# Performance work log

Hardware: AMD Instinct MI355X
Metric: run time of the kernel (lower is better)

## Reference

```python
import jax, jax.numpy as jnp
import numpy as np

N_R = 20          # cfg['n_r']
H = 0.01          # cfg['h'] integration step
ALPHA_N = 0.1     # alpha(D_s_n, R_s_n) folded scale (stable: |eig(H*matAn)| << 2.8)
ALPHA_P = 0.08    # alpha(D_s_p, R_s_p)
BETA_N = -0.5     # -beta(...) for negative electrode
BETA_P = 0.4      # beta(...) for positive electrode


def _make_mats():
    n = N_R - 1
    # FDM tridiagonal (1,-2,1) radial diffusion stencil (spm_model.matA)
    matA = (jnp.diag(-2.0 * jnp.ones(n))
            + jnp.diag(jnp.ones(n - 1), 1)
            + jnp.diag(jnp.ones(n - 1), -1)).astype(jnp.float32)
    # boundary-flux input vector (spm_model.matB): only surface node driven
    matB = jnp.zeros(n, jnp.float32).at[-1].set(1.0)
    matAn = ALPHA_N * matA
    matBn = ALPHA_N * BETA_N * matB
    matAp = ALPHA_P * matA
    matBp = ALPHA_P * BETA_P * matB
    return matAn, matBn, matAp, matBp


def setup_inputs() -> dict:
    key = jax.random.key(0)
    k1, k2 = jax.random.split(key)
    n = N_R - 1
    B, K = 4096, 1024
    x = jax.random.normal(k1, (B, 2 * n), jnp.float32)
    i_seq = jax.random.normal(k2, (B, K), jnp.float32)
    matAn, matBn, matAp, matBp = _make_mats()
    return {"x": x, "i_seq": i_seq,
            "matAn": matAn, "matBn": matBn,
            "matAp": matAp, "matBp": matBp,
            "k": K}


def _rk4_step(x, i_col, A, Bv):
    # f(x) = A @ x + B * i  (batched: x [B,n], i_col [B,1], Bv [n])
    def f(y):
        return y @ A.T + i_col * Bv
    k1 = f(x)
    k2 = f(x + 0.5 * H * k1)
    k3 = f(x + 0.5 * H * k2)
    k4 = f(x + H * k3)
    return x + (H / 6.0) * (k1 + 2.0 * k2 + 2.0 * k3 + k4)


def reference(x, i_seq, matAn, matBn, matAp, matBp, k):
    n = N_R - 1
    xn0, xp0 = x[:, :n], x[:, n:]

    def step(carry, i_t):
        xn, xp = carry
        i_col = i_t[:, None]                      # [B,1]
        xn = _rk4_step(xn, i_col, matAn, matBn)
        xp = _rk4_step(xp, i_col, matAp, matBp)
        return (xn, xp), jnp.concatenate([xn, xp], axis=1)  # [B, 2n]

    _, x_all = jax.lax.scan(step, (xn0, xp0), i_seq.T)      # [k, B, 2n]
    return jnp.transpose(x_all, (1, 2, 0))                  # [B, 2n, k]
```

## Files before the change

kernel.cpp:

```cpp
#include <hip/hip_runtime.h>

#define NCOMP 19
#define NB    4096

typedef float f32x2 __attribute__((ext_vector_type(2)));
typedef float f32x4 __attribute__((ext_vector_type(4)));

constexpr float S20[21] = {
  0.0f, 0.15643446504023087f, 0.3090169943749474f, 0.45399049973954675f,
  0.5877852522924731f, 0.7071067811865476f, 0.8090169943749475f,
  0.8910065241883679f, 0.9510565162951535f, 0.9876883405951378f, 1.0f,
  0.9876883405951378f, 0.9510565162951535f, 0.8910065241883679f,
  0.8090169943749475f, 0.7071067811865476f, 0.5877852522924731f,
  0.45399049973954675f, 0.3090169943749474f, 0.15643446504023087f, 0.0f};

__host__ __device__ constexpr float sval(int m) {
  return (m <= 20) ? S20[m] : -S20[m - 20];
}
__host__ __device__ constexpr float vconst(int k, int j) {
  return sval(((k + 1) * (j + 1)) % 40) * 0.31622776601683794f;
}

struct Tabs { float v[NCOMP][NCOMP]; float lam[NCOMP]; };
__host__ __device__ constexpr Tabs make_tabs() {
  Tabs T{};
  for (int k = 0; k < NCOMP; ++k) {
    for (int j = 0; j < NCOMP; ++j) T.v[k][j] = vconst(k, j);
    T.lam[k] = -2.0f * (1.0f - sval((k + 11) % 40));
  }
  return T;
}
__constant__ Tabs VT = make_tabs();

template <int CTRL, int RMASK>
__device__ __forceinline__ float dpp_add(float x) {
  int v = __builtin_amdgcn_update_dpp(0, __float_as_int(x), CTRL, RMASK, 0xf, true);
  return x + __int_as_float(v);
}
__device__ __forceinline__ float wave_iscan(float x) {
  x = dpp_add<0x111, 0xf>(x);
  x = dpp_add<0x112, 0xf>(x);
  x = dpp_add<0x114, 0xf>(x);
  x = dpp_add<0x118, 0xf>(x);
  x = dpp_add<0x142, 0xa>(x);
  x = dpp_add<0x143, 0xc>(x);
  return x;
}

__global__ __launch_bounds__(256) void spm_fused(
    const float* __restrict__ xin, const float* __restrict__ iseq,
    const float* __restrict__ An, const float* __restrict__ Bn,
    const float* __restrict__ Ap, const float* __restrict__ Bp,
    float* __restrict__ out)
{
  __shared__ float xs0[NCOMP];
  __shared__ float4 mcv[NCOMP];
  __shared__ float2 mgw[NCOMP];
  __shared__ __align__(16) float wtot[NCOMP][4];

  const int t = threadIdx.x;
  const int lane = t & 63, wid = t >> 6;
  const int b = blockIdx.x >> 1, sys = blockIdx.x & 1;
  const float alpha = sys ? Ap[1] : An[1];
  const float ha    = 0.01f * alpha;

  const float4 iv = *reinterpret_cast<const float4*>(iseq + (size_t)b * 1024 + t * 4);

  if (t < NCOMP) xs0[t] = xin[(size_t)b * (2 * NCOMP) + sys * NCOMP + t];
  __syncthreads();

  if (t < NCOMP) {
    float ab = sys ? Bp[NCOMP - 1] : Bn[NCOMP - 1];
    float z  = ha * VT.lam[t];
    float g  = 1.0f + z * (1.0f + z * (0.5f + z * ((1.0f/6.0f) + z * (1.0f/24.0f))));
    float S  = 1.0f + z * (0.5f + z * ((1.0f/6.0f) + z * (1.0f/24.0f)));
    float gi = 1.0f / g;
    float w  = 0.01f * S * ab * VT.v[t][NCOMP - 1];
    float s0 = 0.0f;
#pragma unroll
    for (int j = 0; j < NCOMP; ++j) s0 = fmaf(VT.v[t][j], xs0[j], s0);
    mcv[t] = make_float4(gi, w * gi, __builtin_log2f(g), s0);
    mgw[t] = make_float2(g, w);
  }
  __syncthreads();

  const float pos = (float)(4 * t);

  float Cp[NCOMP];
#pragma unroll
  for (int k = 0; k < NCOMP; ++k) {
    const float4 c = mcv[k];
    float r = iv.x + c.x * (iv.y + c.x * (iv.z + c.x * iv.w));
    float a = __builtin_exp2f(-pos * c.z) * r;
    float v = wave_iscan(a);
    if (lane == 63) wtot[k][wid] = v;
    Cp[k] = v - a;
  }
  __syncthreads();

  f32x2 s01[NCOMP], s23[NCOMP];
#pragma unroll
  for (int k = 0; k < NCOMP; ++k) {
    const float4 c = mcv[k];
    const float2 gw = mgw[k];
    float4 q = *reinterpret_cast<const float4*>(&wtot[k][0]);
    float C = Cp[k];
    if (wid > 0) C += q.x;
    if (wid > 1) C += q.y;
    if (wid > 2) C += q.z;
    float s  = __builtin_exp2f(pos * c.z) * fmaf(c.y, C, c.w);
    float sA = fmaf(gw.x, s,  gw.y * iv.x);
    float sB = fmaf(gw.x, sA, gw.y * iv.y);
    float sC = fmaf(gw.x, sB, gw.y * iv.z);
    float sD = fmaf(gw.x, sC, gw.y * iv.w);
    s01[k] = (f32x2){sA, sB};
    s23[k] = (f32x2){sC, sD};
  }

  f32x4 ob[NCOMP];
#pragma unroll
  for (int jj = 0; jj < 9; ++jj) {
    f32x2 E01 = {0.f, 0.f}, E23 = {0.f, 0.f};
    f32x2 O01 = {0.f, 0.f}, O23 = {0.f, 0.f};
#pragma unroll
    for (int k = 0; k < NCOMP; k += 2) {
      const f32x2 vk = { vconst(k, jj), vconst(k, jj) };
      E01 = __builtin_elementwise_fma(s01[k], vk, E01);
      E23 = __builtin_elementwise_fma(s23[k], vk, E23);
    }
#pragma unroll
    for (int k = 1; k < NCOMP; k += 2) {
      const f32x2 vk = { vconst(k, jj), vconst(k, jj) };
      O01 = __builtin_elementwise_fma(s01[k], vk, O01);
      O23 = __builtin_elementwise_fma(s23[k], vk, O23);
    }
    f32x2 p01 = E01 + O01, p23 = E23 + O23;
    f32x2 m01 = E01 - O01, m23 = E23 - O23;
    ob[jj]      = (f32x4){p01.x, p01.y, p23.x, p23.y};
    ob[18 - jj] = (f32x4){m01.x, m01.y, m23.x, m23.y};
  }
  {
    f32x2 E01 = {0.f, 0.f}, E23 = {0.f, 0.f};
#pragma unroll
    for (int k = 0; k < NCOMP; k += 2) {
      const f32x2 vk = { vconst(k, 9), vconst(k, 9) };
      E01 = __builtin_elementwise_fma(s01[k], vk, E01);
      E23 = __builtin_elementwise_fma(s23[k], vk, E23);
    }
    ob[9] = (f32x4){E01.x, E01.y, E23.x, E23.y};
  }

  float* orow = out + ((size_t)b * (2 * NCOMP) + sys * NCOMP) * 1024 + t * 4;
#pragma unroll
  for (int j = 0; j < NCOMP; ++j)
    __builtin_nontemporal_store(ob[j], reinterpret_cast<f32x4*>(orow + (size_t)j * 1024));
}

extern "C" void kernel_launch(void* const* d_in, const int* in_sizes, int n_in,
                              void* d_out, int out_size, void* d_ws, size_t ws_size,
                              hipStream_t stream) {
  const float* x    = (const float*)d_in[0];
  const float* iseq = (const float*)d_in[1];
  const float* An   = (const float*)d_in[2];
  const float* Bn   = (const float*)d_in[3];
  const float* Ap   = (const float*)d_in[4];
  const float* Bp   = (const float*)d_in[5];
  float* out = (float*)d_out;

  spm_fused<<<NB * 2, 256, 0, stream>>>(x, iseq, An, Bn, Ap, Bp, out);
}
```

Baseline: 127.9 us.

## Make blocks persistent over four batch-system pairs with swizzled block mapping

The grid shrinks from 8192 to 2048 blocks, and each block loops over four (batch, system) pairs. Per-system coefficients are computed once per block for both systems. The initial projection s0 is now computed per lane and broadcast with readlane, which removes an LDS stage and one barrier. The LDS scan totals are double-buffered by iteration parity so one barrier per iteration suffices, and __syncthreads is replaced by a custom waitcnt+s_barrier; the goal is to amortise block setup and launch overhead and to improve write locality through the block swizzle, at the cost of less parallelism and possible tail imbalance.

```diff
diff --git a/kernel.cpp b/kernel.cpp
--- a/kernel.cpp
+++ b/kernel.cpp
@@ -47,113 +47,133 @@
   return x;
 }
 
+__device__ __forceinline__ void lds_barrier() {
+  asm volatile("s_waitcnt lgkmcnt(0)" ::: "memory");
+  __builtin_amdgcn_s_barrier();
+  __builtin_amdgcn_sched_barrier(0);
+}
+
+__device__ __forceinline__ float readlane_f(float v, int k) {
+  return __int_as_float(__builtin_amdgcn_readlane(__float_as_int(v), k));
+}
+
 __global__ __launch_bounds__(256) void spm_fused(
     const float* __restrict__ xin, const float* __restrict__ iseq,
     const float* __restrict__ An, const float* __restrict__ Bn,
     const float* __restrict__ Ap, const float* __restrict__ Bp,
     float* __restrict__ out)
 {
-  __shared__ float xs0[NCOMP];
-  __shared__ float4 mcv[NCOMP];
-  __shared__ float2 mgw[NCOMP];
-  __shared__ __align__(16) float wtot[NCOMP][4];
+  __shared__ float4 mcv[2][NCOMP];
+  __shared__ float  mwv[2][NCOMP];
+  __shared__ __align__(16) float wtot[2][NCOMP][4];
 
   const int t = threadIdx.x;
   const int lane = t & 63, wid = t >> 6;
-  const int b = blockIdx.x >> 1, sys = blockIdx.x & 1;
-  const float alpha = sys ? Ap[1] : An[1];
-  const float ha    = 0.01f * alpha;
+  const int blk = blockIdx.x;
+  const int swz = (blk & 7) * 256 + (blk >> 3);
+  const int pair0 = swz * 4;
 
-  const float4 iv = *reinterpret_cast<const float4*>(iseq + (size_t)b * 1024 + t * 4);
-
-  if (t < NCOMP) xs0[t] = xin[(size_t)b * (2 * NCOMP) + sys * NCOMP + t];
-  __syncthreads();
-
-  if (t < NCOMP) {
-    float ab = sys ? Bp[NCOMP - 1] : Bn[NCOMP - 1];
-    float z  = ha * VT.lam[t];
+  if (t < 2 * NCOMP) {
+    int sy = t / NCOMP, k = t % NCOMP;
+    float alpha = sy ? Ap[1] : An[1];
+    float ab    = sy ? Bp[NCOMP - 1] : Bn[NCOMP - 1];
+    float ha = 0.01f * alpha;
+    float z  = ha * VT.lam[k];
     float g  = 1.0f + z * (1.0f + z * (0.5f + z * ((1.0f/6.0f) + z * (1.0f/24.0f))));
     float S  = 1.0f + z * (0.5f + z * ((1.0f/6.0f) + z * (1.0f/24.0f)));
     float gi = 1.0f / g;
-    float w  = 0.01f * S * ab * VT.v[t][NCOMP - 1];
-    float s0 = 0.0f;
-#pragma unroll
-    for (int j = 0; j < NCOMP; ++j) s0 = fmaf(VT.v[t][j], xs0[j], s0);
-    mcv[t] = make_float4(gi, w * gi, __builtin_log2f(g), s0);
-    mgw[t] = make_float2(g, w);
+    float w  = 0.01f * S * ab * VT.v[k][NCOMP - 1];
+    mcv[sy][k] = make_float4(gi, w * gi, __builtin_log2f(g), g);
+    mwv[sy][k] = w;
   }
-  __syncthreads();
+  lds_barrier();
 
   const float pos = (float)(4 * t);
 
-  float Cp[NCOMP];
+  for (int it = 0; it < 4; ++it) {
+    const int pair = pair0 + it;
+    const int b = pair >> 1, sys = pair & 1;
+    const int par = it & 1;
+
+    const float4 iv = *reinterpret_cast<const float4*>(iseq + (size_t)b * 1024 + t * 4);
+
+    float s0v = 0.0f;
+    if (lane < NCOMP) {
+      const float* xr = xin + (size_t)b * (2 * NCOMP) + sys * NCOMP;
 #pragma unroll
-  for (int k = 0; k < NCOMP; ++k) {
-    const float4 c = mcv[k];
-    float r = iv.x + c.x * (iv.y + c.x * (iv.z + c.x * iv.w));
-    float a = __builtin_exp2f(-pos * c.z) * r;
-    float v = wave_iscan(a);
-    if (lane == 63) wtot[k][wid] = v;
-    Cp[k] = v - a;
+      for (int j = 0; j < NCOMP; ++j) s0v = fmaf(VT.v[lane][j], xr[j], s0v);
+    }
+
+    float Cp[NCOMP];
+#pragma unroll
+    for (int k = 0; k < NCOMP; ++k) {
+      const float4 c = mcv[sys][k];
+      float r = iv.x + c.x * (iv.y + c.x * (iv.z + c.x * iv.w));
+      float a = __builtin_exp2f(-pos * c.z) * r;
+      float v = wave_iscan(a);
+      if (lane == 63) wtot[par][k][wid] = v;
+      Cp[k] = v - a;
+    }
+    lds_barrier();
+
+    f32x2 s01[NCOMP], s23[NCOMP];
+#pragma unroll
+    for (int k = 0; k < NCOMP; ++k) {
+      const float4 c = mcv[sys][k];
+      const float wk = mwv[sys][k];
+      float4 q = *reinterpret_cast<const float4*>(&wtot[par][k][0]);
+      float C = Cp[k];
+      if (wid > 0) C += q.x;
+      if (wid > 1) C += q.y;
+      if (wid > 2) C += q.z;
+      float s0k = readlane_f(s0v, k);
+      float s  = __builtin_exp2f(pos * c.z) * fmaf(c.y, C, s0k);
+      float sA = fmaf(c.w, s,  wk * iv.x);
+      float sB = fmaf(c.w, sA, wk * iv.y);
+      float sC = fmaf(c.w, sB, wk * iv.z);
+      float sD = fmaf(c.w, sC, wk * iv.w);
+      s01[k] = (f32x2){sA, sB};
+      s23[k] = (f32x2){sC, sD};
+    }
+
+    f32x4 ob[NCOMP];
+#pragma unroll
+    for (int jj = 0; jj < 9; ++jj) {
+      f32x2 E01 = {0.f, 0.f}, E23 = {0.f, 0.f};
+      f32x2 O01 = {0.f, 0.f}, O23 = {0.f, 0.f};
+#pragma unroll
+      for (int k = 0; k < NCOMP; k += 2) {
+        const f32x2 vk = { vconst(k, jj), vconst(k, jj) };
+        E01 = __builtin_elementwise_fma(s01[k], vk, E01);
+        E23 = __builtin_elementwise_fma(s23[k], vk, E23);
+      }
+#pragma unroll
+      for (int k = 1; k < NCOMP; k += 2) {
+        const f32x2 vk = { vconst(k, jj), vconst(k, jj) };
+        O01 = __builtin_elementwise_fma(s01[k], vk, O01);
+        O23 = __builtin_elementwise_fma(s23[k], vk, O23);
+      }
+      f32x2 p01 = E01 + O01, p23 = E23 + O23;
+      f32x2 m01 = E01 - O01, m23 = E23 - O23;
+      ob[jj]      = (f32x4){p01.x, p01.y, p23.x, p23.y};
+      ob[18 - jj] = (f32x4){m01.x, m01.y, m23.x, m23.y};
+    }
+    {
+      f32x2 E01 = {0.f, 0.f}, E23 = {0.f, 0.f};
+#pragma unroll
+      for (int k = 0; k < NCOMP; k += 2) {
+        const f32x2 vk = { vconst(k, 9), vconst(k, 9) };
+        E01 = __builtin_elementwise_fma(s01[k], vk, E01);
+        E23 = __builtin_elementwise_fma(s23[k], vk, E23);
+      }
+      ob[9] = (f32x4){E01.x, E01.y, E23.x, E23.y};
+    }
+
+    float* orow = out + ((size_t)b * (2 * NCOMP) + sys * NCOMP) * 1024 + t * 4;
+#pragma unroll
+    for (int j = 0; j < NCOMP; ++j)
+      __builtin_nontemporal_store(ob[j], reinterpret_cast<f32x4*>(orow + (size_t)j * 1024));
   }
-  __syncthreads();
-
-  f32x2 s01[NCOMP], s23[NCOMP];
-#pragma unroll
-  for (int k = 0; k < NCOMP; ++k) {
-    const float4 c = mcv[k];
-    const float2 gw = mgw[k];
-    float4 q = *reinterpret_cast<const float4*>(&wtot[k][0]);
-    float C = Cp[k];
-    if (wid > 0) C += q.x;
-    if (wid > 1) C += q.y;
-    if (wid > 2) C += q.z;
-    float s  = __builtin_exp2f(pos * c.z) * fmaf(c.y, C, c.w);
-    float sA = fmaf(gw.x, s,  gw.y * iv.x);
-    float sB = fmaf(gw.x, sA, gw.y * iv.y);
-    float sC = fmaf(gw.x, sB, gw.y * iv.z);
-    float sD = fmaf(gw.x, sC, gw.y * iv.w);
-    s01[k] = (f32x2){sA, sB};
-    s23[k] = (f32x2){sC, sD};
-  }
-
-  f32x4 ob[NCOMP];
-#pragma unroll
-  for (int jj = 0; jj < 9; ++jj) {
-    f32x2 E01 = {0.f, 0.f}, E23 = {0.f, 0.f};
-    f32x2 O01 = {0.f, 0.f}, O23 = {0.f, 0.f};
-#pragma unroll
-    for (int k = 0; k < NCOMP; k += 2) {
-      const f32x2 vk = { vconst(k, jj), vconst(k, jj) };
-      E01 = __builtin_elementwise_fma(s01[k], vk, E01);
-      E23 = __builtin_elementwise_fma(s23[k], vk, E23);
-    }
-#pragma unroll
-    for (int k = 1; k < NCOMP; k += 2) {
-      const f32x2 vk = { vconst(k, jj), vconst(k, jj) };
-      O01 = __builtin_elementwise_fma(s01[k], vk, O01);
-      O23 = __builtin_elementwise_fma(s23[k], vk, O23);
-    }
-    f32x2 p01 = E01 + O01, p23 = E23 + O23;
-    f32x2 m01 = E01 - O01, m23 = E23 - O23;
-    ob[jj]      = (f32x4){p01.x, p01.y, p23.x, p23.y};
-    ob[18 - jj] = (f32x4){m01.x, m01.y, m23.x, m23.y};
-  }
-  {
-    f32x2 E01 = {0.f, 0.f}, E23 = {0.f, 0.f};
-#pragma unroll
-    for (int k = 0; k < NCOMP; k += 2) {
-      const f32x2 vk = { vconst(k, 9), vconst(k, 9) };
-      E01 = __builtin_elementwise_fma(s01[k], vk, E01);
-      E23 = __builtin_elementwise_fma(s23[k], vk, E23);
-    }
-    ob[9] = (f32x4){E01.x, E01.y, E23.x, E23.y};
-  }
-
-  float* orow = out + ((size_t)b * (2 * NCOMP) + sys * NCOMP) * 1024 + t * 4;
-#pragma unroll
-  for (int j = 0; j < NCOMP; ++j)
-    __builtin_nontemporal_store(ob[j], reinterpret_cast<f32x4*>(orow + (size_t)j * 1024));
 }
 
 extern "C" void kernel_launch(void* const* d_in, const int* in_sizes, int n_in,
@@ -167,5 +187,5 @@
   const float* Bp   = (const float*)d_in[5];
   float* out = (float*)d_out;
 
-  spm_fused<<<NB * 2, 256, 0, stream>>>(x, iseq, An, Bn, Ap, Bp, out);
+  spm_fused<<<2048, 256, 0, stream>>>(x, iseq, An, Bn, Ap, Bp, out);
 }
```

Measured after the change: 133.5 us. +4.4%, slower.
